# Optimization experiments

Measured on AMD Instinct MI355X. Metric: run time of the kernel, lower is better.

The kernel has to match this reference:

```python
import jax, jax.numpy as jnp
import numpy as np

COST_BBOX = 1.0
COST_GIOU = 1.0
TOPK = 5


def _make_boxes(key, b, n):
    # valid xyxy boxes in [0,1]: centers + small positive sizes
    kc, ks = jax.random.split(key)
    cxy = jax.random.uniform(kc, (b, n, 2))
    wh = jax.random.uniform(ks, (b, n, 2)) * 0.2 + 0.01
    return jnp.concatenate([cxy - wh / 2, cxy + wh / 2], axis=-1)


def setup_inputs() -> dict:
    key = jax.random.key(0)
    k1, k2, k3, k4 = jax.random.split(key, 4)
    B, NP, NG = 8, 5000, 300
    return {
        "pred_box": _make_boxes(k1, B, NP),
        "pred_obj": jax.random.normal(k3, (B, NP), dtype=jnp.float32),
        "gt_box": _make_boxes(k2, B, NG),
        "gt_obj": jax.random.normal(k4, (B, NG), dtype=jnp.float32),
    }


def pairwise_giou(pb, gb):
    # pb: [B,N,4], gb: [B,M,4] in xyxy -> giou [B,N,M]
    area_p = (pb[..., 2] - pb[..., 0]) * (pb[..., 3] - pb[..., 1])  # [B,N]
    area_g = (gb[..., 2] - gb[..., 0]) * (gb[..., 3] - gb[..., 1])  # [B,M]
    lt = jnp.maximum(pb[:, :, None, :2], gb[:, None, :, :2])  # [B,N,M,2]
    rb = jnp.minimum(pb[:, :, None, 2:], gb[:, None, :, 2:])
    wh = jnp.clip(rb - lt, 0.0)
    inter = wh[..., 0] * wh[..., 1]                                  # [B,N,M]
    union = area_p[:, :, None] + area_g[:, None, :] - inter
    iou = inter / union
    # smallest enclosing box
    lt_e = jnp.minimum(pb[:, :, None, :2], gb[:, None, :, :2])
    rb_e = jnp.maximum(pb[:, :, None, 2:], gb[:, None, :, 2:])
    wh_e = jnp.clip(rb_e - lt_e, 0.0)
    area_e = wh_e[..., 0] * wh_e[..., 1]
    return iou - (area_e - union) / area_e


def cost_matrix(pred_box, gt_box):
    # L1 cdist: [B,N,M]
    cost_bbox = jnp.sum(jnp.abs(pred_box[:, :, None, :] - gt_box[:, None, :, :]), axis=-1)
    cost_giou = 1.0 - pairwise_giou(pred_box, gt_box)
    return COST_BBOX * cost_bbox + COST_GIOU * cost_giou


def reference(pred_box, pred_obj, gt_box, gt_obj):
    C = cost_matrix(pred_box, gt_box)            # [B, N_pred, N_gt]
    Ct = jnp.swapaxes(C, 1, 2)                   # [B, N_gt, N_pred]
    _, idx = jax.lax.top_k(-Ct, TOPK)            # smallest-cost preds per gt: [B, N_gt, TOPK]
    B, M, _ = idx.shape
    matched_pred = idx.reshape(B, M * TOPK).astype(jnp.int32)
    matched_gt = jnp.broadcast_to(jnp.repeat(jnp.arange(M, dtype=jnp.int32), TOPK)[None, :], (B, M * TOPK))
    return matched_pred, matched_gt
```

## Files before the change

kernel.cpp:

```cpp
#include <hip/hip_runtime.h>

#pragma clang fp contract(off)

typedef unsigned long long u64;

#define TOPK 5
#define WAVES 4

#define CE(x, y) do { if ((y) < (x)) { u64 _t = (x); (x) = (y); (y) = _t; } } while (0)

__device__ __forceinline__ u64 make_key(const float4 pb, const float4 gb,
                                        const float g_area, const int p) {
    const float area_p = (pb.z - pb.x) * (pb.w - pb.y);
    const float cost_bbox = fabsf(pb.x - gb.x) + fabsf(pb.y - gb.y)
                          + fabsf(pb.z - gb.z) + fabsf(pb.w - gb.w);
    const float ltx = fmaxf(pb.x, gb.x), lty = fmaxf(pb.y, gb.y);
    const float rbx = fminf(pb.z, gb.z), rby = fminf(pb.w, gb.w);
    const float iw = fmaxf(rbx - ltx, 0.0f), ih = fmaxf(rby - lty, 0.0f);
    const float inter = iw * ih;
    const float uni = area_p + g_area - inter;
    const float iou = inter / uni;
    const float ex1 = fminf(pb.x, gb.x), ey1 = fminf(pb.y, gb.y);
    const float ex2 = fmaxf(pb.z, gb.z), ey2 = fmaxf(pb.w, gb.w);
    const float ew = fmaxf(ex2 - ex1, 0.0f), eh = fmaxf(ey2 - ey1, 0.0f);
    const float area_e = ew * eh;
    const float giou = iou - (area_e - uni) / area_e;
    const float cost = cost_bbox + (1.0f - giou);
    return ((u64)__float_as_uint(cost) << 32) | (unsigned)p;
}

#define INSERT(nk)                                              \
    do { if ((nk) < k4) {                                       \
        if ((nk) < k3) { k4 = k3;                               \
            if ((nk) < k2) { k3 = k2;                           \
                if ((nk) < k1) { k2 = k1;                       \
                    if ((nk) < k0) { k1 = k0; k0 = (nk); }      \
                    else           { k1 = (nk); }               \
                } else { k2 = (nk); }                           \
            } else { k3 = (nk); }                               \
        } else { k4 = (nk); }                                   \
    } } while (0)

__global__ __launch_bounds__(64 * WAVES) void matcher_topk_kernel(
    const float* __restrict__ pred_box,
    const float* __restrict__ gt_box,
    int* __restrict__ out_pred,
    int* __restrict__ out_gt,
    int B, int NP, int NG)
{
    const int task = blockIdx.x;
    const int wid  = threadIdx.x >> 6;
    const int lane = threadIdx.x & 63;
    const int b = task / NG;
    const int m = task - b * NG;

    const float4 gb = ((const float4*)gt_box)[b * NG + m];
    const float g_area = (gb.z - gb.x) * (gb.w - gb.y);

    u64 k0 = ~0ULL, k1 = ~0ULL, k2 = ~0ULL, k3 = ~0ULL, k4 = ~0ULL;

    const float4* pbase = (const float4*)pred_box + (size_t)b * NP;
    const int stride = 64 * WAVES;

    int p = wid * 64 + lane;
    for (; p + stride < NP; p += 2 * stride) {
        const float4 pa = pbase[p];
        const float4 pc = pbase[p + stride];
        const u64 ka = make_key(pa, gb, g_area, p);
        const u64 kc = make_key(pc, gb, g_area, p + stride);
        INSERT(ka);
        INSERT(kc);
    }
    if (p < NP) {
        const float4 pa = pbase[p];
        const u64 ka = make_key(pa, gb, g_area, p);
        INSERT(ka);
    }

    #pragma unroll
    for (int off = 1; off < 64; off <<= 1) {
        const u64 b0 = __shfl_xor(k0, off);
        const u64 b1 = __shfl_xor(k1, off);
        const u64 b2 = __shfl_xor(k2, off);
        const u64 b3 = __shfl_xor(k3, off);
        const u64 b4 = __shfl_xor(k4, off);
        u64 m0 = k0 < b4 ? k0 : b4;
        u64 m1 = k1 < b3 ? k1 : b3;
        u64 m2 = k2 < b2 ? k2 : b2;
        u64 m3 = k3 < b1 ? k3 : b1;
        u64 m4 = k4 < b0 ? k4 : b0;
        CE(m0, m1); CE(m3, m4); CE(m2, m4); CE(m2, m3); CE(m1, m4);
        CE(m0, m3); CE(m0, m2); CE(m1, m3); CE(m1, m2);
        k0 = m0; k1 = m1; k2 = m2; k3 = m3; k4 = m4;
    }

    __shared__ u64 lds[WAVES][TOPK];
    if (lane == 0) {
        lds[wid][0] = k0; lds[wid][1] = k1; lds[wid][2] = k2;
        lds[wid][3] = k3; lds[wid][4] = k4;
    }
    __syncthreads();

    if (threadIdx.x == 0) {
        int head[WAVES];
        #pragma unroll
        for (int w = 0; w < WAVES; ++w) head[w] = 0;
        const int base = task * TOPK;
        #pragma unroll
        for (int r = 0; r < TOPK; ++r) {
            u64 best = ~0ULL; int bw = 0;
            #pragma unroll
            for (int w = 0; w < WAVES; ++w) {
                const u64 v = lds[w][head[w]];
                if (v < best) { best = v; bw = w; }
            }
            head[bw]++;
            out_pred[base + r] = (int)(unsigned)(best & 0xFFFFFFFFu);
            out_gt[base + r]   = m;
        }
    }
}

extern "C" void kernel_launch(void* const* d_in, const int* in_sizes, int n_in,
                              void* d_out, int out_size, void* d_ws, size_t ws_size,
                              hipStream_t stream) {
    const float* pred_box = (const float*)d_in[0];
    const float* gt_box   = (const float*)d_in[2];

    const int NP = 5000;
    const int B  = in_sizes[1] / NP;
    const int NG = in_sizes[3] / B;

    int* out_pred = (int*)d_out;
    int* out_gt   = out_pred + B * NG * TOPK;

    const int total = B * NG;
    hipLaunchKernelGGL(matcher_topk_kernel, dim3(total), dim3(64 * WAVES), 0, stream,
                       pred_box, gt_box, out_pred, out_gt, B, NP, NG);
}
```

Measured before the change: 42.50 us.

## Process two GT boxes per block and use fast reciprocal division

Each block now handles a pair of ground-truth boxes, so every loaded prediction box and its area are reused for two cost evaluations, with a separate top-5 list kept per GT. This halves the grid size and cuts the redundant pred loads and area computations. The IEEE divide is replaced by a hardware reciprocal plus Newton refinement, and the clamp on the enclosing box width is removed. Register pressure and shuffle work per wave double, and the approximate divide could change tie ordering in rare cases.

```diff
diff --git a/kernel.cpp b/kernel.cpp
--- a/kernel.cpp
+++ b/kernel.cpp
@@ -9,27 +9,7 @@
 
 #define CE(x, y) do { if ((y) < (x)) { u64 _t = (x); (x) = (y); (y) = _t; } } while (0)
 
-__device__ __forceinline__ u64 make_key(const float4 pb, const float4 gb,
-                                        const float g_area, const int p) {
-    const float area_p = (pb.z - pb.x) * (pb.w - pb.y);
-    const float cost_bbox = fabsf(pb.x - gb.x) + fabsf(pb.y - gb.y)
-                          + fabsf(pb.z - gb.z) + fabsf(pb.w - gb.w);
-    const float ltx = fmaxf(pb.x, gb.x), lty = fmaxf(pb.y, gb.y);
-    const float rbx = fminf(pb.z, gb.z), rby = fminf(pb.w, gb.w);
-    const float iw = fmaxf(rbx - ltx, 0.0f), ih = fmaxf(rby - lty, 0.0f);
-    const float inter = iw * ih;
-    const float uni = area_p + g_area - inter;
-    const float iou = inter / uni;
-    const float ex1 = fminf(pb.x, gb.x), ey1 = fminf(pb.y, gb.y);
-    const float ex2 = fmaxf(pb.z, gb.z), ey2 = fmaxf(pb.w, gb.w);
-    const float ew = fmaxf(ex2 - ex1, 0.0f), eh = fmaxf(ey2 - ey1, 0.0f);
-    const float area_e = ew * eh;
-    const float giou = iou - (area_e - uni) / area_e;
-    const float cost = cost_bbox + (1.0f - giou);
-    return ((u64)__float_as_uint(cost) << 32) | (unsigned)p;
-}
-
-#define INSERT(nk)                                              \
+#define INSERT(nk, k0, k1, k2, k3, k4)                          \
     do { if ((nk) < k4) {                                       \
         if ((nk) < k3) { k4 = k3;                               \
             if ((nk) < k2) { k3 = k2;                           \
@@ -41,6 +21,33 @@
         } else { k4 = (nk); }                                   \
     } } while (0)
 
+__device__ __forceinline__ float fast_div(float a, float b) {
+    float r = __builtin_amdgcn_rcpf(b);
+    r = fmaf(fmaf(-b, r, 1.0f), r, r);
+    float q = a * r;
+    q = fmaf(fmaf(-b, q, a), r, q);
+    return q;
+}
+
+__device__ __forceinline__ u64 eval_key(const float4 pb, const float area_p,
+                                        const float4 gb, const float g_area,
+                                        const int p) {
+    const float cost_bbox = fabsf(pb.x - gb.x) + fabsf(pb.y - gb.y)
+                          + fabsf(pb.z - gb.z) + fabsf(pb.w - gb.w);
+    const float ltx = fmaxf(pb.x, gb.x), lty = fmaxf(pb.y, gb.y);
+    const float rbx = fminf(pb.z, gb.z), rby = fminf(pb.w, gb.w);
+    const float iw = fmaxf(rbx - ltx, 0.0f), ih = fmaxf(rby - lty, 0.0f);
+    const float inter = iw * ih;
+    const float uni = area_p + g_area - inter;
+    const float iou = fast_div(inter, uni);
+    const float ex1 = fminf(pb.x, gb.x), ey1 = fminf(pb.y, gb.y);
+    const float ex2 = fmaxf(pb.z, gb.z), ey2 = fmaxf(pb.w, gb.w);
+    const float area_e = (ex2 - ex1) * (ey2 - ey1);
+    const float giou = iou - fast_div(area_e - uni, area_e);
+    const float cost = cost_bbox + (1.0f - giou);
+    return ((u64)__float_as_uint(cost) << 32) | (unsigned)p;
+}
+
 __global__ __launch_bounds__(64 * WAVES) void matcher_topk_kernel(
     const float* __restrict__ pred_box,
     const float* __restrict__ gt_box,
@@ -48,75 +55,112 @@
     int* __restrict__ out_gt,
     int B, int NP, int NG)
 {
-    const int task = blockIdx.x;
+    const int pairsPerB = (NG + 1) >> 1;
+    const int tp = blockIdx.x;
+    const int b  = tp / pairsPerB;
+    const int j  = tp - b * pairsPerB;
+    const int m0 = 2 * j;
+    const int m1 = m0 + 1;
+    const bool has1 = (m1 < NG);
+
     const int wid  = threadIdx.x >> 6;
     const int lane = threadIdx.x & 63;
-    const int b = task / NG;
-    const int m = task - b * NG;
 
-    const float4 gb = ((const float4*)gt_box)[b * NG + m];
-    const float g_area = (gb.z - gb.x) * (gb.w - gb.y);
+    const float4 gb0 = ((const float4*)gt_box)[b * NG + m0];
+    const float4 gb1 = ((const float4*)gt_box)[b * NG + (has1 ? m1 : m0)];
+    const float ga0 = (gb0.z - gb0.x) * (gb0.w - gb0.y);
+    const float ga1 = (gb1.z - gb1.x) * (gb1.w - gb1.y);
 
-    u64 k0 = ~0ULL, k1 = ~0ULL, k2 = ~0ULL, k3 = ~0ULL, k4 = ~0ULL;
+    u64 a0 = ~0ULL, a1 = ~0ULL, a2 = ~0ULL, a3 = ~0ULL, a4 = ~0ULL;
+    u64 c0 = ~0ULL, c1 = ~0ULL, c2 = ~0ULL, c3 = ~0ULL, c4 = ~0ULL;
 
     const float4* pbase = (const float4*)pred_box + (size_t)b * NP;
-    const int stride = 64 * WAVES;
 
-    int p = wid * 64 + lane;
-    for (; p + stride < NP; p += 2 * stride) {
-        const float4 pa = pbase[p];
-        const float4 pc = pbase[p + stride];
-        const u64 ka = make_key(pa, gb, g_area, p);
-        const u64 kc = make_key(pc, gb, g_area, p + stride);
-        INSERT(ka);
-        INSERT(kc);
+    int p = threadIdx.x;
+    for (; p + 256 < NP; p += 512) {
+        const float4 pA = pbase[p];
+        const float4 pB = pbase[p + 256];
+        const float apA = (pA.z - pA.x) * (pA.w - pA.y);
+        const float apB = (pB.z - pB.x) * (pB.w - pB.y);
+        const u64 kA0 = eval_key(pA, apA, gb0, ga0, p);
+        const u64 kB0 = eval_key(pB, apB, gb0, ga0, p + 256);
+        const u64 kA1 = eval_key(pA, apA, gb1, ga1, p);
+        const u64 kB1 = eval_key(pB, apB, gb1, ga1, p + 256);
+        INSERT(kA0, a0, a1, a2, a3, a4);
+        INSERT(kB0, a0, a1, a2, a3, a4);
+        INSERT(kA1, c0, c1, c2, c3, c4);
+        INSERT(kB1, c0, c1, c2, c3, c4);
     }
     if (p < NP) {
-        const float4 pa = pbase[p];
-        const u64 ka = make_key(pa, gb, g_area, p);
-        INSERT(ka);
+        const float4 pA = pbase[p];
+        const float apA = (pA.z - pA.x) * (pA.w - pA.y);
+        const u64 kA0 = eval_key(pA, apA, gb0, ga0, p);
+        const u64 kA1 = eval_key(pA, apA, gb1, ga1, p);
+        INSERT(kA0, a0, a1, a2, a3, a4);
+        INSERT(kA1, c0, c1, c2, c3, c4);
     }
 
     #pragma unroll
     for (int off = 1; off < 64; off <<= 1) {
-        const u64 b0 = __shfl_xor(k0, off);
-        const u64 b1 = __shfl_xor(k1, off);
-        const u64 b2 = __shfl_xor(k2, off);
-        const u64 b3 = __shfl_xor(k3, off);
-        const u64 b4 = __shfl_xor(k4, off);
-        u64 m0 = k0 < b4 ? k0 : b4;
-        u64 m1 = k1 < b3 ? k1 : b3;
-        u64 m2 = k2 < b2 ? k2 : b2;
-        u64 m3 = k3 < b1 ? k3 : b1;
-        u64 m4 = k4 < b0 ? k4 : b0;
-        CE(m0, m1); CE(m3, m4); CE(m2, m4); CE(m2, m3); CE(m1, m4);
-        CE(m0, m3); CE(m0, m2); CE(m1, m3); CE(m1, m2);
-        k0 = m0; k1 = m1; k2 = m2; k3 = m3; k4 = m4;
+        const u64 sa0 = __shfl_xor(a0, off);
+        const u64 sa1 = __shfl_xor(a1, off);
+        const u64 sa2 = __shfl_xor(a2, off);
+        const u64 sa3 = __shfl_xor(a3, off);
+        const u64 sa4 = __shfl_xor(a4, off);
+        const u64 sc0 = __shfl_xor(c0, off);
+        const u64 sc1 = __shfl_xor(c1, off);
+        const u64 sc2 = __shfl_xor(c2, off);
+        const u64 sc3 = __shfl_xor(c3, off);
+        const u64 sc4 = __shfl_xor(c4, off);
+
+        u64 x0 = a0 < sa4 ? a0 : sa4;
+        u64 x1 = a1 < sa3 ? a1 : sa3;
+        u64 x2 = a2 < sa2 ? a2 : sa2;
+        u64 x3 = a3 < sa1 ? a3 : sa1;
+        u64 x4 = a4 < sa0 ? a4 : sa0;
+        CE(x0, x1); CE(x3, x4); CE(x2, x4); CE(x2, x3); CE(x1, x4);
+        CE(x0, x3); CE(x0, x2); CE(x1, x3); CE(x1, x2);
+        a0 = x0; a1 = x1; a2 = x2; a3 = x3; a4 = x4;
+
+        u64 y0 = c0 < sc4 ? c0 : sc4;
+        u64 y1 = c1 < sc3 ? c1 : sc3;
+        u64 y2 = c2 < sc2 ? c2 : sc2;
+        u64 y3 = c3 < sc1 ? c3 : sc1;
+        u64 y4 = c4 < sc0 ? c4 : sc0;
+        CE(y0, y1); CE(y3, y4); CE(y2, y4); CE(y2, y3); CE(y1, y4);
+        CE(y0, y3); CE(y0, y2); CE(y1, y3); CE(y1, y2);
+        c0 = y0; c1 = y1; c2 = y2; c3 = y3; c4 = y4;
     }
 
-    __shared__ u64 lds[WAVES][TOPK];
+    __shared__ u64 lds[2][WAVES][TOPK];
     if (lane == 0) {
-        lds[wid][0] = k0; lds[wid][1] = k1; lds[wid][2] = k2;
-        lds[wid][3] = k3; lds[wid][4] = k4;
+        lds[0][wid][0] = a0; lds[0][wid][1] = a1; lds[0][wid][2] = a2;
+        lds[0][wid][3] = a3; lds[0][wid][4] = a4;
+        lds[1][wid][0] = c0; lds[1][wid][1] = c1; lds[1][wid][2] = c2;
+        lds[1][wid][3] = c3; lds[1][wid][4] = c4;
     }
     __syncthreads();
 
-    if (threadIdx.x == 0) {
-        int head[WAVES];
-        #pragma unroll
-        for (int w = 0; w < WAVES; ++w) head[w] = 0;
-        const int base = task * TOPK;
-        #pragma unroll
-        for (int r = 0; r < TOPK; ++r) {
-            u64 best = ~0ULL; int bw = 0;
+    if (threadIdx.x < 2) {
+        const int which = threadIdx.x;
+        if (which == 0 || has1) {
+            const int m = m0 + which;
+            int head[WAVES];
             #pragma unroll
-            for (int w = 0; w < WAVES; ++w) {
-                const u64 v = lds[w][head[w]];
-                if (v < best) { best = v; bw = w; }
+            for (int w = 0; w < WAVES; ++w) head[w] = 0;
+            const int base = (b * NG + m) * TOPK;
+            #pragma unroll
+            for (int r = 0; r < TOPK; ++r) {
+                u64 best = ~0ULL; int bw = 0;
+                #pragma unroll
+                for (int w = 0; w < WAVES; ++w) {
+                    const u64 v = lds[which][w][head[w]];
+                    if (v < best) { best = v; bw = w; }
+                }
+                head[bw]++;
+                out_pred[base + r] = (int)(unsigned)(best & 0xFFFFFFFFu);
+                out_gt[base + r]   = m;
             }
-            head[bw]++;
-            out_pred[base + r] = (int)(unsigned)(best & 0xFFFFFFFFu);
-            out_gt[base + r]   = m;
         }
     }
 }
@@ -134,7 +178,8 @@
     int* out_pred = (int*)d_out;
     int* out_gt   = out_pred + B * NG * TOPK;
 
-    const int total = B * NG;
-    hipLaunchKernelGGL(matcher_topk_kernel, dim3(total), dim3(64 * WAVES), 0, stream,
+    const int pairsPerB = (NG + 1) >> 1;
+    const int blocks = B * pairsPerB;
+    hipLaunchKernelGGL(matcher_topk_kernel, dim3(blocks), dim3(64 * WAVES), 0, stream,
                        pred_box, gt_box, out_pred, out_gt, B, NP, NG);
 }
```

Measured after the change: 40.44 us. 1.05x faster.
